# Performance work log

Hardware: AMD Instinct MI355X
Metric: run time of the kernel (lower is better)

## Reference

```python
import jax, jax.numpy as jnp
import numpy as np

DIM = 1024
D_STATE = 16
D_CONV = 4
EXPAND = 2
D_INNER = EXPAND * DIM          # 2048
DT_RANK = (DIM + 15) // 16      # 64 (math.ceil(d_model/16))
BSZ = 2
SEQ = 2048


def setup_inputs() -> dict:
    key = jax.random.key(0)
    ks = jax.random.split(key, 8)
    g = lambda k, shape, scale: (jax.random.normal(k, shape, jnp.float32) * scale)
    return {
        "x": g(ks[0], (BSZ, SEQ, DIM), 1.0),
        # in_proj: Linear(d_model -> 2*d_inner, bias=False)
        "W_in": g(ks[1], (2 * D_INNER, DIM), DIM ** -0.5),
        # depthwise causal conv1d: groups=d_inner, kernel d_conv, bias=True
        "conv_w": g(ks[2], (D_INNER, 1, D_CONV), D_CONV ** -0.5),
        "conv_b": jnp.zeros((D_INNER,), jnp.float32),
        # x_proj: Linear(d_inner -> dt_rank + 2*d_state, bias=False)
        "W_xproj": g(ks[3], (DT_RANK + 2 * D_STATE, D_INNER), D_INNER ** -0.5),
        # dt_proj: Linear(dt_rank -> d_inner, bias=True)
        "W_dt": g(ks[4], (D_INNER, DT_RANK), DT_RANK ** -0.5),
        "b_dt": g(ks[5], (D_INNER,), 0.1),
        # S4D-real init: A = -exp(A_log), A_log = log(1..d_state)
        "A_log": jnp.log(jnp.broadcast_to(
            jnp.arange(1, D_STATE + 1, dtype=jnp.float32), (D_INNER, D_STATE))),
        "D": jnp.ones((D_INNER,), jnp.float32),
        # out_proj: Linear(d_inner -> d_model, bias=False)
        "W_out": g(ks[6], (DIM, D_INNER), D_INNER ** -0.5),
        # wrapper LayerNorm(dim)
        "gamma": jnp.ones((DIM,), jnp.float32),
        "beta": jnp.zeros((DIM,), jnp.float32),
    }


def reference(x, W_in, conv_w, conv_b, W_xproj, W_dt, b_dt,
              A_log, D, W_out, gamma, beta):
    B, L, _ = x.shape
    # ---- input projection, split into conv path and gate ----
    xz = x @ W_in.T                              # (B, L, 2*d_inner)
    xc, z = jnp.split(xz, 2, axis=-1)
    # ---- depthwise causal conv1d + SiLU ----
    xt = jnp.transpose(xc, (0, 2, 1))            # (B, d_inner, L)
    conv = jax.lax.conv_general_dilated(
        xt, conv_w, window_strides=(1,), padding=[(D_CONV - 1, 0)],
        dimension_numbers=("NCH", "OIH", "NCH"), feature_group_count=D_INNER)
    u = jax.nn.silu(jnp.transpose(conv + conv_b[None, :, None], (0, 2, 1)))  # (B,L,d_inner)
    # ---- input-dependent delta, B, C ----
    xdbc = u @ W_xproj.T                          # (B, L, dt_rank + 2*d_state)
    dt = xdbc[..., :DT_RANK]
    Bm = xdbc[..., DT_RANK:DT_RANK + D_STATE]     # (B, L, d_state)
    Cm = xdbc[..., DT_RANK + D_STATE:]            # (B, L, d_state)
    delta = jax.nn.softplus(dt @ W_dt.T + b_dt)   # (B, L, d_inner)
    A = -jnp.exp(A_log)                           # (d_inner, d_state)
    # ---- selective scan: h_t = exp(dt*A) h_{t-1} + dt*B_t*u_t ; y_t = <h_t, C_t> ----
    def step(h, inputs):
        d_t, u_t, B_t, C_t = inputs               # (B,d_inner),(B,d_inner),(B,S),(B,S)
        dA = jnp.exp(d_t[:, :, None] * A)         # (B, d_inner, S)
        h = h * dA + (d_t * u_t)[:, :, None] * B_t[:, None, :]
        y = jnp.einsum("bds,bs->bd", h, C_t)
        return h, y
    tm = lambda a: jnp.transpose(a, (1, 0, 2))    # time-major for scan
    h0 = jnp.zeros((B, D_INNER, D_STATE), x.dtype)
    _, ys = jax.lax.scan(step, h0, (tm(delta), tm(u), tm(Bm), tm(Cm)))
    y = jnp.transpose(ys, (1, 0, 2)) + u * D      # skip term D*u
    y = y * jax.nn.silu(z)                        # gate
    out = y @ W_out.T                             # (B, L, dim)
    # ---- wrapper LayerNorm(dim), eps=1e-5 ----
    mean = out.mean(-1, keepdims=True)
    var = out.var(-1, keepdims=True)
    return (out - mean) * jax.lax.rsqrt(var + 1e-5) * gamma + beta
```

## Files before the change

kernel.cpp:

```cpp
#include <hip/hip_runtime.h>
#include <stdint.h>

typedef unsigned short u16;
typedef __bf16 bf16x8 __attribute__((ext_vector_type(8)));
typedef unsigned short u16x8 __attribute__((ext_vector_type(8)));
typedef unsigned short u16x4 __attribute__((ext_vector_type(4)));
typedef float f32x4 __attribute__((ext_vector_type(4)));

#define BSZ 2
#define SEQ 2048
#define DIM 1024
#define D_INNER 2048
#define DT_RANK 64
#define D_STATE 16
#define XPROJ_N 96
#define NCHUNK 32
#define CHUNK_T 64
#define LOG2E 1.44269504f

#define N_X   4194304
#define N_W   4194304
#define N_WX  196608
#define N_WDT 131072
#define N_WO  2097152
#define N_XD  393216

__device__ __forceinline__ float bf2f(u16 h) {
    return __uint_as_float(((unsigned)h) << 16);
}
__device__ __forceinline__ u16 f2bf(float f) {
    unsigned u = __float_as_uint(f);
    unsigned r = (u + 0x7FFFu + ((u >> 16) & 1u)) >> 16;
    return (u16)r;
}

__device__ __forceinline__ f32x4 mfma16(bf16x8 a, bf16x8 b, f32x4 c) {
    return __builtin_amdgcn_mfma_f32_16x16x32_bf16(a, b, c, 0, 0, 0);
}

__device__ __forceinline__ void gload_lds16(const void* g, void* l) {
    __builtin_amdgcn_global_load_lds(
        (const __attribute__((address_space(1))) unsigned int*)(uintptr_t)g,
        (__attribute__((address_space(3))) unsigned int*)(uintptr_t)l,
        16, 0, 0);
}

__device__ __forceinline__ void split4(const float* __restrict__ in,
                                       u16* __restrict__ hi, u16* __restrict__ lo,
                                       long i)
{
    f32x4 v = *(const f32x4*)(in + i);
    u16x4 h, l;
    #pragma unroll
    for (int j = 0; j < 4; j++) {
        u16 hh = f2bf(v[j]);
        h[j] = hh;
        l[j] = f2bf(v[j] - bf2f(hh));
    }
    *(u16x4*)(hi + i) = h;
    *(u16x4*)(lo + i) = l;
}

__global__ __launch_bounds__(256)
void megasplit4(const float* __restrict__ x,  u16* __restrict__ xh,  u16* __restrict__ xl,
                const float* __restrict__ w,  u16* __restrict__ wh,  u16* __restrict__ wl,
                const float* __restrict__ wx, u16* __restrict__ wxh, u16* __restrict__ wxl,
                const float* __restrict__ wd, u16* __restrict__ wdh, u16* __restrict__ wdl)
{
    long i = ((long)blockIdx.x * 256 + threadIdx.x) * 4;
    if (i < N_X) { split4(x, xh, xl, i); return; }
    i -= N_X;
    if (i < N_W) { split4(w, wh, wl, i); return; }
    i -= N_W;
    if (i < N_WX) { split4(wx, wxh, wxl, i); return; }
    i -= N_WX;
    if (i < N_WDT) { split4(wd, wdh, wdl, i); }
}

#define PH_TOP                                                                \
    __builtin_amdgcn_sched_barrier(0);                                        \
    __builtin_amdgcn_s_barrier();                                             \
    asm volatile("s_waitcnt lgkmcnt(0)" ::: "memory");                        \
    __builtin_amdgcn_sched_barrier(0);                                        \
    __builtin_amdgcn_s_setprio(1);
#define PH_BOT                                                                \
    __builtin_amdgcn_s_setprio(0);                                            \
    __builtin_amdgcn_sched_barrier(0);                                        \
    __builtin_amdgcn_s_barrier();

__global__ __launch_bounds__(512, 2)
void gemm256_xz(const u16* __restrict__ xh, const u16* __restrict__ xl,
                const u16* __restrict__ wh, const u16* __restrict__ wl,
                u16* __restrict__ xc, float* __restrict__ z)
{
    __shared__ u16 lds[65536];

    const int tid  = threadIdx.x;
    const int w    = tid >> 6;
    const int lane = tid & 63;
    const int r16  = lane & 15;
    const int quad = lane >> 4;
    const int wr   = w >> 2;
    const int wc   = w & 3;
    const long m0  = (long)blockIdx.y * 256;
    const long n0  = (long)blockIdx.x * 256;

    const int c0 = tid, c1 = tid + 512;
    const int ma0 = c0 >> 2, kc0 = ((c0 & 3) ^ ((ma0 >> 1) & 3)) * 8;
    const int ma1 = c1 >> 2, kc1 = ((c1 & 3) ^ ((ma1 >> 1) & 3)) * 8;
    const int arow0 = ((int)m0 + ma0) * DIM + kc0;
    const int arow1 = ((int)m0 + ma1) * DIM + kc1;
    const int brow0 = ((int)n0 + ma0) * DIM + kc0;
    const int brow1 = ((int)n0 + ma1) * DIM + kc1;

    int caof[8], cbof[4];
    #pragma unroll
    for (int i = 0; i < 8; i++) {
        int m = wr * 128 + i * 16 + r16;
        caof[i] = (m * 4 + (quad ^ ((m >> 1) & 3))) * 8;
    }
    #pragma unroll
    for (int j = 0; j < 4; j++) {
        int n = wc * 64 + j * 16 + r16;
        cbof[j] = (n * 4 + (quad ^ ((n >> 1) & 3))) * 8;
    }

    f32x4 acc[8][4];
    #pragma unroll
    for (int i = 0; i < 8; i++)
        #pragma unroll
        for (int j = 0; j < 4; j++) acc[i][j] = {0.f, 0.f, 0.f, 0.f};

    gload_lds16(xh + arow0, lds + c0 * 8);
    gload_lds16(xh + arow1, lds + c1 * 8);
    gload_lds16(xl + arow0, lds + 8192 + c0 * 8);
    gload_lds16(xl + arow1, lds + 8192 + c1 * 8);
    gload_lds16(wh + brow0, lds + 16384 + c0 * 8);
    gload_lds16(wh + brow1, lds + 16384 + c1 * 8);
    gload_lds16(wl + brow0, lds + 24576 + c0 * 8);
    gload_lds16(wl + brow1, lds + 24576 + c1 * 8);
    asm volatile("s_waitcnt vmcnt(0)" ::: "memory");
    __builtin_amdgcn_s_barrier();

    int kt = 0;
#define XZ_FTILE(CUR, SN)                                                     \
  {                                                                           \
    int st = kt + 1; if (st > 31) st = 31;                                    \
    const int kb = st * 32;                                                   \
    const u16* AHp = lds + (CUR) * 32768;                                     \
    const u16* ALp = AHp + 8192;                                              \
    const u16* BHp = AHp + 16384;                                             \
    const u16* BLp = AHp + 24576;                                             \
    u16* Sb = lds + (SN) * 32768;                                             \
    bf16x8 a0[4], a1[4], fb[4];                                               \
                            \
    _Pragma("unroll") for (int j = 0; j < 4; j++)                             \
        fb[j] = *(const bf16x8*)(BHp + cbof[j]);                              \
    _Pragma("unroll") for (int i = 0; i < 4; i++)                             \
        a0[i] = *(const bf16x8*)(AHp + caof[i]);                              \
    gload_lds16(xh + arow0 + kb, Sb + c0 * 8);                                \
    gload_lds16(xh + arow1 + kb, Sb + c1 * 8);                                \
    PH_TOP                                                                    \
    _Pragma("unroll") for (int i = 0; i < 4; i++)                             \
      _Pragma("unroll") for (int j = 0; j < 4; j++)                           \
        acc[i][j] = mfma16(a0[i], fb[j], acc[i][j]);                          \
    PH_BOT                                                                    \
                                \
    _Pragma("unroll") for (int i = 0; i < 4; i++)                             \
        a1[i] = *(const bf16x8*)(AHp + caof[4 + i]);                          \
    gload_lds16(xl + arow0 + kb, Sb + 8192 + c0 * 8);                         \
    gload_lds16(xl + arow1 + kb, Sb + 8192 + c1 * 8);                         \
    PH_TOP                                                                    \
    _Pragma("unroll") for (int i = 0; i < 4; i++)                             \
      _Pragma("unroll") for (int j = 0; j < 4; j++)                           \
        acc[4 + i][j] = mfma16(a1[i], fb[j], acc[4 + i][j]);                  \
    PH_BOT                                                                    \
                        \
    _Pragma("unroll") for (int j = 0; j < 4; j++)                             \
        fb[j] = *(const bf16x8*)(BLp + cbof[j]);                              \
    gload_lds16(wh + brow0 + kb, Sb + 16384 + c0 * 8);                        \
    gload_lds16(wh + brow1 + kb, Sb + 16384 + c1 * 8);                        \
    PH_TOP                                                                    \
    _Pragma("unroll") for (int i = 0; i < 4; i++)                             \
      _Pragma("unroll") for (int j = 0; j < 4; j++)                           \
        acc[i][j] = mfma16(a0[i], fb[j], acc[i][j]);                          \
    PH_BOT                                                                    \
                             \
    gload_lds16(wl + brow0 + kb, Sb + 24576 + c0 * 8);                        \
    gload_lds16(wl + brow1 + kb, Sb + 24576 + c1 * 8);                        \
    PH_TOP                                                                    \
    _Pragma("unroll") for (int i = 0; i < 4; i++)                             \
      _Pragma("unroll") for (int j = 0; j < 4; j++)                           \
        acc[4 + i][j] = mfma16(a1[i], fb[j], acc[4 + i][j]);                  \
    PH_BOT                                                                    \
                              \
    _Pragma("unroll") for (int j = 0; j < 4; j++)                             \
        fb[j] = *(const bf16x8*)(BHp + cbof[j]);                              \
    _Pragma("unroll") for (int i = 0; i < 4; i++)                             \
        a0[i] = *(const bf16x8*)(ALp + caof[i]);                              \
    PH_TOP                                                                    \
    _Pragma("unroll") for (int i = 0; i < 4; i++)                             \
      _Pragma("unroll") for (int j = 0; j < 4; j++)                           \
        acc[i][j] = mfma16(a0[i], fb[j], acc[i][j]);                          \
    PH_BOT                                                                    \
                 \
    _Pragma("unroll") for (int i = 0; i < 4; i++)                             \
        a1[i] = *(const bf16x8*)(ALp + caof[4 + i]);                          \
    PH_TOP                                                                    \
    _Pragma("unroll") for (int i = 0; i < 4; i++)                             \
      _Pragma("unroll") for (int j = 0; j < 4; j++)                           \
        acc[4 + i][j] = mfma16(a1[i], fb[j], acc[4 + i][j]);                  \
    __builtin_amdgcn_s_setprio(0);                                            \
    __builtin_amdgcn_sched_barrier(0);                                        \
    asm volatile("s_waitcnt vmcnt(0)" ::: "memory");                          \
    __builtin_amdgcn_s_barrier();                                             \
    kt++;                                                                     \
  }

    #pragma unroll 1
    for (int it = 0; it < 16; it++) {
        XZ_FTILE(0, 1)
        XZ_FTILE(1, 0)
    }
#undef XZ_FTILE

    asm volatile("s_waitcnt vmcnt(0)" ::: "memory");

    const bool isz = (n0 >= 2048);
    #pragma unroll
    for (int i = 0; i < 8; i++) {
        #pragma unroll
        for (int j = 0; j < 4; j++) {
            long col = n0 + wc * 64 + j * 16 + r16;
            #pragma unroll
            for (int r = 0; r < 4; r++) {
                long row = m0 + wr * 128 + i * 16 + quad * 4 + r;
                if (!isz) xc[row * (long)D_INNER + col] = f2bf(acc[i][j][r]);
                else      z[row * (long)D_INNER + (col - D_INNER)] = acc[i][j][r];
            }
        }
    }
}

__global__ __launch_bounds__(512, 2)
void gemm256_out(const u16* __restrict__ A, const u16* __restrict__ Bh,
                 const u16* __restrict__ Bl, float* __restrict__ OutBase)
{
    __shared__ u16 lds[49152];

    const int tid  = threadIdx.x;
    const int w    = tid >> 6;
    const int lane = tid & 63;
    const int r16  = lane & 15;
    const int quad = lane >> 4;
    const int wr   = w >> 2;
    const int wc   = w & 3;
    const long m0  = (long)blockIdx.y * 256;
    const long n0  = (long)blockIdx.x * 256;
    const int  kz  = blockIdx.z;
    const u16* Bs  = (kz >= 2) ? Bl : Bh;
    const int  kbase = (kz & 1) * 1024;
    float* Out = OutBase + (long)kz * 4194304;

    const int c0 = tid, c1 = tid + 512;
    const int ma0 = c0 >> 2, kc0 = ((c0 & 3) ^ ((ma0 >> 1) & 3)) * 8;
    const int ma1 = c1 >> 2, kc1 = ((c1 & 3) ^ ((ma1 >> 1) & 3)) * 8;
    const int arow0 = ((int)m0 + ma0) * D_INNER + kbase + kc0;
    const int arow1 = ((int)m0 + ma1) * D_INNER + kbase + kc1;
    const int brow0 = ((int)n0 + ma0) * D_INNER + kbase + kc0;
    const int brow1 = ((int)n0 + ma1) * D_INNER + kbase + kc1;

    int caof[8], cbof[4];
    #pragma unroll
    for (int i = 0; i < 8; i++) {
        int m = wr * 128 + i * 16 + r16;
        caof[i] = (m * 4 + (quad ^ ((m >> 1) & 3))) * 8;
    }
    #pragma unroll
    for (int j = 0; j < 4; j++) {
        int n = wc * 64 + j * 16 + r16;
        cbof[j] = (n * 4 + (quad ^ ((n >> 1) & 3))) * 8;
    }

    f32x4 acc[8][4];
    #pragma unroll
    for (int i = 0; i < 8; i++)
        #pragma unroll
        for (int j = 0; j < 4; j++) acc[i][j] = {0.f, 0.f, 0.f, 0.f};

    gload_lds16(A  + arow0,      lds + c0 * 8);
    gload_lds16(A  + arow1,      lds + c1 * 8);
    gload_lds16(Bs + brow0,      lds + 24576 + c0 * 8);
    gload_lds16(Bs + brow1,      lds + 24576 + c1 * 8);
    gload_lds16(A  + arow0 + 32, lds + 8192 + c0 * 8);
    gload_lds16(A  + arow1 + 32, lds + 8192 + c1 * 8);
    gload_lds16(Bs + brow0 + 32, lds + 24576 + 8192 + c0 * 8);
    gload_lds16(Bs + brow1 + 32, lds + 24576 + 8192 + c1 * 8);
    asm volatile("s_waitcnt vmcnt(4)" ::: "memory");
    __builtin_amdgcn_s_barrier();

    int kt = 0;
#define OUT_ITER(CUR, SL)                                                     \
  {                                                                           \
    int st = kt + 2; if (st > 31) st = 31;                                    \
    const int kb = st * 32;                                                   \
    const u16* Alds = lds + (CUR) * 8192;                                     \
    const u16* Blds = lds + 24576 + (CUR) * 8192;                             \
    bf16x8 bfr[4], afr[4];                                                    \
    _Pragma("unroll") for (int j = 0; j < 4; j++)                             \
        bfr[j] = *(const bf16x8*)(Blds + cbof[j]);                            \
    _Pragma("unroll") for (int i = 0; i < 4; i++)                             \
        afr[i] = *(const bf16x8*)(Alds + caof[i]);                            \
    gload_lds16(A + arow0 + kb, lds + (SL) * 8192 + c0 * 8);                  \
    gload_lds16(A + arow1 + kb, lds + (SL) * 8192 + c1 * 8);                  \
    PH_TOP                                                                    \
    _Pragma("unroll") for (int i = 0; i < 4; i++)                             \
      _Pragma("unroll") for (int j = 0; j < 4; j++)                           \
        acc[i][j] = mfma16(afr[i], bfr[j], acc[i][j]);                        \
    PH_BOT                                                                    \
    bf16x8 af2[4];                                                            \
    _Pragma("unroll") for (int i = 0; i < 4; i++)                             \
        af2[i] = *(const bf16x8*)(Alds + caof[4 + i]);                        \
    gload_lds16(Bs + brow0 + kb, lds + 24576 + (SL) * 8192 + c0 * 8);         \
    gload_lds16(Bs + brow1 + kb, lds + 24576 + (SL) * 8192 + c1 * 8);         \
    PH_TOP                                                                    \
    _Pragma("unroll") for (int i = 0; i < 4; i++)                             \
      _Pragma("unroll") for (int j = 0; j < 4; j++)                           \
        acc[4 + i][j] = mfma16(af2[i], bfr[j], acc[4 + i][j]);                \
    __builtin_amdgcn_s_setprio(0);                                            \
    __builtin_amdgcn_sched_barrier(0);                                        \
    asm volatile("s_waitcnt vmcnt(4)" ::: "memory");                          \
    __builtin_amdgcn_s_barrier();                                             \
    kt++;                                                                     \
  }

    #pragma unroll 1
    for (int it = 0; it < 10; it++) {
        OUT_ITER(0, 2)
        OUT_ITER(1, 0)
        OUT_ITER(2, 1)
    }
    OUT_ITER(0, 2)
    OUT_ITER(1, 0)
#undef OUT_ITER

    asm volatile("s_waitcnt vmcnt(0)" ::: "memory");

    #pragma unroll
    for (int i = 0; i < 8; i++) {
        #pragma unroll
        for (int j = 0; j < 4; j++) {
            long col = n0 + wc * 64 + j * 16 + r16;
            #pragma unroll
            for (int r = 0; r < 4; r++) {
                long row = m0 + wr * 128 + i * 16 + quad * 4 + r;
                Out[row * (long)DIM + col] = acc[i][j][r];
            }
        }
    }
}

__global__ __launch_bounds__(64)
void gemm_dt32(const u16* __restrict__ Ah, const u16* __restrict__ Al, int lda,
               const u16* __restrict__ Bh, const u16* __restrict__ Bl, int ldb,
               float* __restrict__ C, int ldc, const float* __restrict__ bias)
{
    const int lane = threadIdx.x;
    const int r16  = lane & 15;
    const int quad = lane >> 4;
    const long m0 = (long)blockIdx.y * 32;
    const long n0 = (long)blockIdx.x * 32;

    const u16* Ah0 = Ah + (m0 + r16) * (long)lda + quad * 8;
    const u16* Ah1 = Ah0 + 16L * lda;
    const u16* Al0 = Al + (m0 + r16) * (long)lda + quad * 8;
    const u16* Al1 = Al0 + 16L * lda;
    const u16* Bh0 = Bh + (n0 + r16) * (long)ldb + quad * 8;
    const u16* Bh1 = Bh0 + 16L * ldb;
    const u16* Bl0 = Bl + (n0 + r16) * (long)ldb + quad * 8;
    const u16* Bl1 = Bl0 + 16L * ldb;

    f32x4 acc00 = {0,0,0,0}, acc01 = {0,0,0,0}, acc10 = {0,0,0,0}, acc11 = {0,0,0,0};

    #pragma unroll
    for (int k = 0; k < DT_RANK; k += 32) {
        bf16x8 a0h = *(const bf16x8*)(Ah0 + k);
        bf16x8 a1h = *(const bf16x8*)(Ah1 + k);
        bf16x8 a0l = *(const bf16x8*)(Al0 + k);
        bf16x8 a1l = *(const bf16x8*)(Al1 + k);
        bf16x8 b0h = *(const bf16x8*)(Bh0 + k);
        bf16x8 b1h = *(const bf16x8*)(Bh1 + k);
        bf16x8 b0l = *(const bf16x8*)(Bl0 + k);
        bf16x8 b1l = *(const bf16x8*)(Bl1 + k);
        acc00 = mfma16(a0h, b0h, acc00); acc00 = mfma16(a0h, b0l, acc00); acc00 = mfma16(a0l, b0h, acc00);
        acc01 = mfma16(a0h, b1h, acc01); acc01 = mfma16(a0h, b1l, acc01); acc01 = mfma16(a0l, b1h, acc01);
        acc10 = mfma16(a1h, b0h, acc10); acc10 = mfma16(a1h, b0l, acc10); acc10 = mfma16(a1l, b0h, acc10);
        acc11 = mfma16(a1h, b1h, acc11); acc11 = mfma16(a1h, b1l, acc11); acc11 = mfma16(a1l, b1h, acc11);
    }

    #pragma unroll
    for (int i = 0; i < 2; i++) {
        #pragma unroll
        for (int j = 0; j < 2; j++) {
            f32x4 v = (i == 0) ? (j == 0 ? acc00 : acc01) : (j == 0 ? acc10 : acc11);
            long col = n0 + j * 16 + r16;
            #pragma unroll
            for (int r = 0; r < 4; r++) {
                long row = m0 + i * 16 + quad * 4 + r;
                float x = v[r] + bias[col];
                x = (x > 15.f) ? x : log1pf(__expf(x));
                C[row * (long)ldc + col] = x;
            }
        }
    }
}

__global__ __launch_bounds__(64)
void gemm3_skp(const u16* __restrict__ A, int lda,
               const u16* __restrict__ Bh, const u16* __restrict__ Bl, int ldb,
               float* __restrict__ Cpart, int ldc, int K0)
{
    const int lane = threadIdx.x;
    const int r16  = lane & 15;
    const int quad = lane >> 4;
    const long m0 = (long)blockIdx.y * 32;
    const long n0 = (long)blockIdx.x * 32;
    const int kbase = blockIdx.z * K0;
    float* C = Cpart + (long)blockIdx.z * N_XD;

    const u16* Ap0 = A  + (m0 + r16) * (long)lda + quad * 8 + kbase;
    const u16* Ap1 = Ap0 + 16L * lda;
    const u16* Bh0 = Bh + (n0 + r16) * (long)ldb + quad * 8 + kbase;
    const u16* Bh1 = Bh0 + 16L * ldb;
    const u16* Bl0 = Bl + (n0 + r16) * (long)ldb + quad * 8 + kbase;
    const u16* Bl1 = Bl0 + 16L * ldb;

    f32x4 acc00 = {0,0,0,0}, acc01 = {0,0,0,0}, acc10 = {0,0,0,0}, acc11 = {0,0,0,0};

    for (int k = 0; k < K0; k += 32) {
        bf16x8 a0 = *(const bf16x8*)(Ap0 + k);
        bf16x8 a1 = *(const bf16x8*)(Ap1 + k);
        bf16x8 b0h = *(const bf16x8*)(Bh0 + k);
        bf16x8 b1h = *(const bf16x8*)(Bh1 + k);
        bf16x8 b0l = *(const bf16x8*)(Bl0 + k);
        bf16x8 b1l = *(const bf16x8*)(Bl1 + k);
        acc00 = mfma16(a0, b0h, acc00); acc00 = mfma16(a0, b0l, acc00);
        acc01 = mfma16(a0, b1h, acc01); acc01 = mfma16(a0, b1l, acc01);
        acc10 = mfma16(a1, b0h, acc10); acc10 = mfma16(a1, b0l, acc10);
        acc11 = mfma16(a1, b1h, acc11); acc11 = mfma16(a1, b1l, acc11);
    }

    #pragma unroll
    for (int i = 0; i < 2; i++) {
        #pragma unroll
        for (int j = 0; j < 2; j++) {
            f32x4 v = (i == 0) ? (j == 0 ? acc00 : acc01) : (j == 0 ? acc10 : acc11);
            long col = n0 + j * 16 + r16;
            #pragma unroll
            for (int r = 0; r < 4; r++) {
                long row = m0 + i * 16 + quad * 4 + r;
                C[row * (long)ldc + col] = v[r];
            }
        }
    }
}

__global__ __launch_bounds__(256)
void combine3(const float* __restrict__ part, float* __restrict__ xdbc,
              u16* __restrict__ hi, u16* __restrict__ lo)
{
    long i = ((long)blockIdx.x * 256 + threadIdx.x) * 4;
    if (i >= N_XD) return;
    f32x4 s = *(const f32x4*)(part + i);
    #pragma unroll
    for (int j = 1; j < 8; j++) {
        f32x4 p = *(const f32x4*)(part + (long)j * N_XD + i);
        s[0] += p[0]; s[1] += p[1]; s[2] += p[2]; s[3] += p[3];
    }
    *(f32x4*)(xdbc + i) = s;
    u16x4 h, l;
    #pragma unroll
    for (int j = 0; j < 4; j++) {
        u16 hh = f2bf(s[j]);
        h[j] = hh;
        l[j] = f2bf(s[j] - bf2f(hh));
    }
    *(u16x4*)(hi + i) = h;
    *(u16x4*)(lo + i) = l;
}

__global__ __launch_bounds__(256)
void conv_silu(const u16* __restrict__ xc, const float* __restrict__ cw,
               const float* __restrict__ cb, u16* __restrict__ u)
{
    long idx = ((long)blockIdx.x * 256 + threadIdx.x) * 8;
    int t  = (int)((idx >> 11) & 2047);
    int d0 = (int)(idx & 2047);

    bf16x8 xrow[4];
    #pragma unroll
    for (int j = 0; j < 4; j++) {
        int tt = t - 3 + j;
        if (tt >= 0) xrow[j] = *(const bf16x8*)(xc + idx + (long)(j - 3) * D_INNER);
        else         xrow[j] = bf16x8{0,0,0,0,0,0,0,0};
    }
    u16x8 out;
    #pragma unroll
    for (int e = 0; e < 8; e++) {
        int d = d0 + e;
        float acc = cb[d];
        #pragma unroll
        for (int j = 0; j < 4; j++)
            acc += cw[d * 4 + j] * (float)xrow[j][e];
        out[e] = f2bf(acc / (1.f + __expf(-acc)));
    }
    *(u16x8*)(u + idx) = out;
}

__global__ __launch_bounds__(256)
void scan_partA(const float* __restrict__ delta, const u16* __restrict__ u,
                const float* __restrict__ xdbc, const float* __restrict__ A_log,
                float* __restrict__ hbuf, float* __restrict__ sdelta,
                const float* __restrict__ wout, u16* __restrict__ wouth,
                u16* __restrict__ woutl)
{
    const int d = blockIdx.x * 256 + threadIdx.x;
    const int c = blockIdx.y;
    const int b = blockIdx.z;
    const int t0 = c * CHUNK_T;

    float Af[16];
    #pragma unroll
    for (int s = 0; s < 16; s++) Af[s] = -__expf(A_log[d * 16 + s]) * LOG2E;
    bool fast = true;
    #pragma unroll
    for (int s = 0; s < 16; s++)
        fast = fast && (fabsf(Af[s] - (float)(s + 1) * Af[0]) < 1e-3f * (float)(s + 1));

    float h[16];
    #pragma unroll
    for (int s = 0; s < 16; s++) h[s] = 0.f;
    float sd = 0.f;

    const float* dptr = delta + ((long)b * SEQ + t0) * D_INNER + d;
    const u16*   uptr = u     + ((long)b * SEQ + t0) * D_INNER + d;
    const float* xp   = xdbc  + ((long)b * SEQ + t0) * XPROJ_N;

    if (fast) {
        const float Af0 = Af[0];
        for (int t = 0; t < CHUNK_T; t++) {
            float dl = dptr[(long)t * D_INNER];
            float uu = bf2f(uptr[(long)t * D_INNER]);
            f32x4 B0 = *(const f32x4*)(xp + t * XPROJ_N + DT_RANK);
            f32x4 B1 = *(const f32x4*)(xp + t * XPROJ_N + DT_RANK + 4);
            f32x4 B2 = *(const f32x4*)(xp + t * XPROJ_N + DT_RANK + 8);
            f32x4 B3 = *(const f32x4*)(xp + t * XPROJ_N + DT_RANK + 12);
            float Bv[16] = {B0[0],B0[1],B0[2],B0[3], B1[0],B1[1],B1[2],B1[3],
                            B2[0],B2[1],B2[2],B2[3], B3[0],B3[1],B3[2],B3[3]};
            sd += dl;
            float dlu = dl * uu;
            float q = exp2f(dl * Af0);
            float dAc = 1.f;
            #pragma unroll
            for (int s = 0; s < 16; s++) {
                dAc *= q;
                h[s] = h[s] * dAc + dlu * Bv[s];
            }
        }
    } else {
        for (int t = 0; t < CHUNK_T; t++) {
            float dl = dptr[(long)t * D_INNER];
            float uu = bf2f(uptr[(long)t * D_INNER]);
            f32x4 B0 = *(const f32x4*)(xp + t * XPROJ_N + DT_RANK);
            f32x4 B1 = *(const f32x4*)(xp + t * XPROJ_N + DT_RANK + 4);
            f32x4 B2 = *(const f32x4*)(xp + t * XPROJ_N + DT_RANK + 8);
            f32x4 B3 = *(const f32x4*)(xp + t * XPROJ_N + DT_RANK + 12);
            float Bv[16] = {B0[0],B0[1],B0[2],B0[3], B1[0],B1[1],B1[2],B1[3],
                            B2[0],B2[1],B2[2],B2[3], B3[0],B3[1],B3[2],B3[3]};
            sd += dl;
            float dlu = dl * uu;
            #pragma unroll
            for (int s = 0; s < 16; s++)
                h[s] = h[s] * exp2f(dl * Af[s]) + dlu * Bv[s];
        }
    }

    float* hout = hbuf + ((long)(b * NCHUNK + c) * D_INNER + d) * 16;
    #pragma unroll
    for (int s = 0; s < 16; s++) hout[s] = h[s];
    sdelta[(long)(b * NCHUNK + c) * D_INNER + d] = sd;

    long tidg = (((long)b * NCHUNK + c) * 8 + blockIdx.x) * 256 + threadIdx.x;
    long base = tidg * 16;
    #pragma unroll
    for (int k = 0; k < 4; k++) split4(wout, wouth, woutl, base + 4 * k);
}

__global__ __launch_bounds__(256)
void scan_fixup(float* __restrict__ hbuf, const float* __restrict__ sdelta,
                const float* __restrict__ A_log)
{
    const int idx = blockIdx.x * 256 + threadIdx.x;
    const int ds = idx & (D_INNER * 16 - 1);
    const int b  = idx >> 15;
    const float Af = -__expf(A_log[ds]) * LOG2E;
    float hin = 0.f;
    #pragma unroll 4
    for (int c = 0; c < NCHUNK; c++) {
        long gi = (long)(b * NCHUNK + c) * (D_INNER * 16) + ds;
        float e = hbuf[gi];
        hbuf[gi] = hin;
        float sd = sdelta[(long)(b * NCHUNK + c) * D_INNER + (ds >> 4)];
        hin = e + exp2f(Af * sd) * hin;
    }
}

__global__ __launch_bounds__(256)
void scan_partC(const float* __restrict__ delta, const u16* __restrict__ u,
                const float* __restrict__ xdbc, const float* __restrict__ z,
                const float* __restrict__ A_log, const float* __restrict__ Dp,
                const float* __restrict__ hbuf, u16* __restrict__ y)
{
    const int d = blockIdx.x * 256 + threadIdx.x;
    const int c = blockIdx.y;
    const int b = blockIdx.z;
    const int t0 = c * CHUNK_T;

    float Af[16];
    #pragma unroll
    for (int s = 0; s < 16; s++) Af[s] = -__expf(A_log[d * 16 + s]) * LOG2E;
    bool fast = true;
    #pragma unroll
    for (int s = 0; s < 16; s++)
        fast = fast && (fabsf(Af[s] - (float)(s + 1) * Af[0]) < 1e-3f * (float)(s + 1));
    const float Dd = Dp[d];

    float h[16];
    const float* hin = hbuf + ((long)(b * NCHUNK + c) * D_INNER + d) * 16;
    #pragma unroll
    for (int s = 0; s < 16; s++) h[s] = hin[s];

    const float* dptr = delta + ((long)b * SEQ + t0) * D_INNER + d;
    const u16*   uptr = u     + ((long)b * SEQ + t0) * D_INNER + d;
    const float* zptr = z     + ((long)b * SEQ + t0) * D_INNER + d;
    const float* xp   = xdbc  + ((long)b * SEQ + t0) * XPROJ_N;
    u16* yptr = y + ((long)b * SEQ + t0) * D_INNER + d;

    if (fast) {
        const float Af0 = Af[0];
        for (int t = 0; t < CHUNK_T; t++) {
            float dl = dptr[(long)t * D_INNER];
            float uu = bf2f(uptr[(long)t * D_INNER]);
            float zl = zptr[(long)t * D_INNER];
            f32x4 B0 = *(const f32x4*)(xp + t * XPROJ_N + DT_RANK);
            f32x4 B1 = *(const f32x4*)(xp + t * XPROJ_N + DT_RANK + 4);
            f32x4 B2 = *(const f32x4*)(xp + t * XPROJ_N + DT_RANK + 8);
            f32x4 B3 = *(const f32x4*)(xp + t * XPROJ_N + DT_RANK + 12);
            f32x4 C0 = *(const f32x4*)(xp + t * XPROJ_N + DT_RANK + 16);
            f32x4 C1 = *(const f32x4*)(xp + t * XPROJ_N + DT_RANK + 20);
            f32x4 C2 = *(const f32x4*)(xp + t * XPROJ_N + DT_RANK + 24);
            f32x4 C3 = *(const f32x4*)(xp + t * XPROJ_N + DT_RANK + 28);
            float Bv[16] = {B0[0],B0[1],B0[2],B0[3], B1[0],B1[1],B1[2],B1[3],
                            B2[0],B2[1],B2[2],B2[3], B3[0],B3[1],B3[2],B3[3]};
            float Cv[16] = {C0[0],C0[1],C0[2],C0[3], C1[0],C1[1],C1[2],C1[3],
                            C2[0],C2[1],C2[2],C2[3], C3[0],C3[1],C3[2],C3[3]};
            float dlu = dl * uu;
            float q = exp2f(dl * Af0);
            float dAc = 1.f;
            float p0 = 0.f, p1 = 0.f, p2 = 0.f, p3 = 0.f;
            #pragma unroll
            for (int s = 0; s < 16; s += 4) {
                float dA0 = dAc * q;
                float dA1 = dA0 * q;
                float dA2 = dA1 * q;
                float dA3 = dA2 * q;
                dAc = dA3;
                h[s]   = h[s]   * dA0 + dlu * Bv[s];
                h[s+1] = h[s+1] * dA1 + dlu * Bv[s+1];
                h[s+2] = h[s+2] * dA2 + dlu * Bv[s+2];
                h[s+3] = h[s+3] * dA3 + dlu * Bv[s+3];
                p0 += h[s]   * Cv[s];
                p1 += h[s+1] * Cv[s+1];
                p2 += h[s+2] * Cv[s+2];
                p3 += h[s+3] * Cv[s+3];
            }
            float acc = (p0 + p1) + (p2 + p3);
            float sz = zl / (1.f + __expf(-zl));
            float yy = (acc + uu * Dd) * sz;
            yptr[(long)t * D_INNER] = f2bf(yy);
        }
    } else {
        for (int t = 0; t < CHUNK_T; t++) {
            float dl = dptr[(long)t * D_INNER];
            float uu = bf2f(uptr[(long)t * D_INNER]);
            float zl = zptr[(long)t * D_INNER];
            f32x4 B0 = *(const f32x4*)(xp + t * XPROJ_N + DT_RANK);
            f32x4 B1 = *(const f32x4*)(xp + t * XPROJ_N + DT_RANK + 4);
            f32x4 B2 = *(const f32x4*)(xp + t * XPROJ_N + DT_RANK + 8);
            f32x4 B3 = *(const f32x4*)(xp + t * XPROJ_N + DT_RANK + 12);
            f32x4 C0 = *(const f32x4*)(xp + t * XPROJ_N + DT_RANK + 16);
            f32x4 C1 = *(const f32x4*)(xp + t * XPROJ_N + DT_RANK + 20);
            f32x4 C2 = *(const f32x4*)(xp + t * XPROJ_N + DT_RANK + 24);
            f32x4 C3 = *(const f32x4*)(xp + t * XPROJ_N + DT_RANK + 28);
            float Bv[16] = {B0[0],B0[1],B0[2],B0[3], B1[0],B1[1],B1[2],B1[3],
                            B2[0],B2[1],B2[2],B2[3], B3[0],B3[1],B3[2],B3[3]};
            float Cv[16] = {C0[0],C0[1],C0[2],C0[3], C1[0],C1[1],C1[2],C1[3],
                            C2[0],C2[1],C2[2],C2[3], C3[0],C3[1],C3[2],C3[3]};
            float dlu = dl * uu;
            float p0 = 0.f, p1 = 0.f, p2 = 0.f, p3 = 0.f;
            #pragma unroll
            for (int s = 0; s < 16; s += 4) {
                h[s]   = h[s]   * exp2f(dl * Af[s])   + dlu * Bv[s];
                h[s+1] = h[s+1] * exp2f(dl * Af[s+1]) + dlu * Bv[s+1];
                h[s+2] = h[s+2] * exp2f(dl * Af[s+2]) + dlu * Bv[s+2];
                h[s+3] = h[s+3] * exp2f(dl * Af[s+3]) + dlu * Bv[s+3];
                p0 += h[s]   * Cv[s];
                p1 += h[s+1] * Cv[s+1];
                p2 += h[s+2] * Cv[s+2];
                p3 += h[s+3] * Cv[s+3];
            }
            float acc = (p0 + p1) + (p2 + p3);
            float sz = zl / (1.f + __expf(-zl));
            float yy = (acc + uu * Dd) * sz;
            yptr[(long)t * D_INNER] = f2bf(yy);
        }
    }
}

__global__ __launch_bounds__(256)
void layernorm_kernel(const float* __restrict__ p0,
                      const float* __restrict__ gamma, const float* __restrict__ beta,
                      float* __restrict__ out)
{
    const long row = blockIdx.x;
    const long base = row * DIM;
    int tid = threadIdx.x;
    float v[4];
    float sum = 0.f, sq = 0.f;
    #pragma unroll
    for (int i = 0; i < 4; i++) {
        long c = base + tid + i * 256;
        v[i] = (p0[c] + p0[c + 4194304]) + (p0[c + 8388608] + p0[c + 12582912]);
        sum += v[i];
        sq  += v[i] * v[i];
    }
    #pragma unroll
    for (int off = 1; off < 64; off <<= 1) {
        sum += __shfl_xor(sum, off);
        sq  += __shfl_xor(sq, off);
    }
    __shared__ float ssum[4], ssq[4];
    int w = tid >> 6;
    if ((tid & 63) == 0) { ssum[w] = sum; ssq[w] = sq; }
    __syncthreads();
    float ts = ssum[0] + ssum[1] + ssum[2] + ssum[3];
    float tq = ssq[0] + ssq[1] + ssq[2] + ssq[3];
    float mean = ts * (1.f / DIM);
    float var  = tq * (1.f / DIM) - mean * mean;
    float rstd = rsqrtf(var + 1e-5f);
    float* o = out + base;
    #pragma unroll
    for (int i = 0; i < 4; i++) {
        int c = tid + i * 256;
        o[c] = (v[i] - mean) * rstd * gamma[c] + beta[c];
    }
}

extern "C" void kernel_launch(void* const* d_in, const int* in_sizes, int n_in,
                              void* d_out, int out_size, void* d_ws, size_t ws_size,
                              hipStream_t stream)
{
    const float* x      = (const float*)d_in[0];
    const float* W_in   = (const float*)d_in[1];
    const float* conv_w = (const float*)d_in[2];
    const float* conv_b = (const float*)d_in[3];
    const float* W_xproj= (const float*)d_in[4];
    const float* W_dt   = (const float*)d_in[5];
    const float* b_dt   = (const float*)d_in[6];
    const float* A_log  = (const float*)d_in[7];
    const float* Dv     = (const float*)d_in[8];
    const float* W_out  = (const float*)d_in[9];
    const float* gamma  = (const float*)d_in[10];
    const float* beta   = (const float*)d_in[11];

    char* ws = (char*)d_ws;
    u16*   xc    = (u16*)(ws);
    float* g3p   = (float*)(ws);
    u16*   xdh   = (u16*)(ws + 12582912);
    u16*   xdl   = (u16*)(ws + 14155776);
    float* hbuf  = (float*)(ws);
    u16*   wouth = (u16*)(ws + 8388608);
    u16*   woutl = (u16*)(ws + 12582912);
    float* z     = (float*)(ws + 16777216);
    float* opre  = (float*)(ws + 16777216);
    u16*   u     = (u16*)(ws + 50331648);
    u16*   xh    = (u16*)(ws + 67108864);
    u16*   xl    = (u16*)(ws + 75497472);
    u16*   wh    = (u16*)(ws + 83886080);
    u16*   wl    = (u16*)(ws + 92274688);
    float* delta = (float*)(ws + 67108864);
    float* xdbc  = (float*)(ws + 100663296);
    u16*   wxh   = (u16*)(ws + 102236160);
    u16*   wxl   = (u16*)(ws + 102629376);
    u16*   wdth  = (u16*)(ws + 103022592);
    u16*   wdtl  = (u16*)(ws + 103284736);
    float* sdel  = (float*)(ws + 103546880);
    u16*   yb    = (u16*)d_out;

    megasplit4<<<8512, 256, 0, stream>>>(x, xh, xl, W_in, wh, wl,
                                         W_xproj, wxh, wxl, W_dt, wdth, wdtl);
    gemm256_xz<<<dim3(16, 16), 512, 0, stream>>>(xh, xl, wh, wl, xc, z);
    conv_silu<<<4096, 256, 0, stream>>>(xc, conv_w, conv_b, u);
    gemm3_skp<<<dim3(3, 128, 8), 64, 0, stream>>>(
        u, D_INNER, wxh, wxl, D_INNER, g3p, XPROJ_N, 256);
    combine3<<<384, 256, 0, stream>>>(g3p, xdbc, xdh, xdl);
    gemm_dt32<<<dim3(64, 128), 64, 0, stream>>>(
        xdh, xdl, XPROJ_N, wdth, wdtl, DT_RANK, delta, D_INNER, b_dt);
    scan_partA<<<dim3(8, NCHUNK, BSZ), 256, 0, stream>>>(
        delta, u, xdbc, A_log, hbuf, sdel, W_out, wouth, woutl);
    scan_fixup<<<256, 256, 0, stream>>>(hbuf, sdel, A_log);
    scan_partC<<<dim3(8, NCHUNK, BSZ), 256, 0, stream>>>(delta, u, xdbc, z, A_log, Dv, hbuf, yb);
    gemm256_out<<<dim3(4, 16, 4), 512, 0, stream>>>(yb, wouth, woutl, opre);
    layernorm_kernel<<<4096, 256, 0, stream>>>(opre, gamma, beta, (float*)d_out);
}
```

Baseline: 391.6 us.

## Restructure out-projection GEMM to share A tile across hi/lo weight halves

The out-projection GEMM previously split K and the hi/lo bf16 weight halves across four z-slices, each loading its own A tile and writing a separate partial sum. It now uses 128-row tiles with two K-split slices, loads the A tile once per stage, and applies it against both Bh and Bl, so A traffic drops and only two partials need summing in LayerNorm. The pipeline depth goes from three stages to two with full vmcnt waits. In the xz GEMM, the hi/lo B fragments are kept in separate registers to avoid reloading Bh from LDS, at the cost of extra VGPRs.

```diff
diff --git a/kernel.cpp b/kernel.cpp
--- a/kernel.cpp
+++ b/kernel.cpp
@@ -152,10 +152,10 @@
     const u16* BHp = AHp + 16384;                                             \
     const u16* BLp = AHp + 24576;                                             \
     u16* Sb = lds + (SN) * 32768;                                             \
-    bf16x8 a0[4], a1[4], fb[4];                                               \
+    bf16x8 a0[4], a1[4], fbh[4], fbl[4];                                      \
                             \
     _Pragma("unroll") for (int j = 0; j < 4; j++)                             \
-        fb[j] = *(const bf16x8*)(BHp + cbof[j]);                              \
+        fbh[j] = *(const bf16x8*)(BHp + cbof[j]);                             \
     _Pragma("unroll") for (int i = 0; i < 4; i++)                             \
         a0[i] = *(const bf16x8*)(AHp + caof[i]);                              \
     gload_lds16(xh + arow0 + kb, Sb + c0 * 8);                                \
@@ -163,7 +163,7 @@
     PH_TOP                                                                    \
     _Pragma("unroll") for (int i = 0; i < 4; i++)                             \
       _Pragma("unroll") for (int j = 0; j < 4; j++)                           \
-        acc[i][j] = mfma16(a0[i], fb[j], acc[i][j]);                          \
+        acc[i][j] = mfma16(a0[i], fbh[j], acc[i][j]);                         \
     PH_BOT                                                                    \
                                 \
     _Pragma("unroll") for (int i = 0; i < 4; i++)                             \
@@ -173,17 +173,17 @@
     PH_TOP                                                                    \
     _Pragma("unroll") for (int i = 0; i < 4; i++)                             \
       _Pragma("unroll") for (int j = 0; j < 4; j++)                           \
-        acc[4 + i][j] = mfma16(a1[i], fb[j], acc[4 + i][j]);                  \
+        acc[4 + i][j] = mfma16(a1[i], fbh[j], acc[4 + i][j]);                 \
     PH_BOT                                                                    \
                         \
     _Pragma("unroll") for (int j = 0; j < 4; j++)                             \
-        fb[j] = *(const bf16x8*)(BLp + cbof[j]);                              \
+        fbl[j] = *(const bf16x8*)(BLp + cbof[j]);                             \
     gload_lds16(wh + brow0 + kb, Sb + 16384 + c0 * 8);                        \
     gload_lds16(wh + brow1 + kb, Sb + 16384 + c1 * 8);                        \
     PH_TOP                                                                    \
     _Pragma("unroll") for (int i = 0; i < 4; i++)                             \
       _Pragma("unroll") for (int j = 0; j < 4; j++)                           \
-        acc[i][j] = mfma16(a0[i], fb[j], acc[i][j]);                          \
+        acc[i][j] = mfma16(a0[i], fbl[j], acc[i][j]);                         \
     PH_BOT                                                                    \
                              \
     gload_lds16(wl + brow0 + kb, Sb + 24576 + c0 * 8);                        \
@@ -191,25 +191,23 @@
     PH_TOP                                                                    \
     _Pragma("unroll") for (int i = 0; i < 4; i++)                             \
       _Pragma("unroll") for (int j = 0; j < 4; j++)                           \
-        acc[4 + i][j] = mfma16(a1[i], fb[j], acc[4 + i][j]);                  \
+        acc[4 + i][j] = mfma16(a1[i], fbl[j], acc[4 + i][j]);                 \
     PH_BOT                                                                    \
-                              \
-    _Pragma("unroll") for (int j = 0; j < 4; j++)                             \
-        fb[j] = *(const bf16x8*)(BHp + cbof[j]);                              \
+                   \
     _Pragma("unroll") for (int i = 0; i < 4; i++)                             \
         a0[i] = *(const bf16x8*)(ALp + caof[i]);                              \
     PH_TOP                                                                    \
     _Pragma("unroll") for (int i = 0; i < 4; i++)                             \
       _Pragma("unroll") for (int j = 0; j < 4; j++)                           \
-        acc[i][j] = mfma16(a0[i], fb[j], acc[i][j]);                          \
+        acc[i][j] = mfma16(a0[i], fbh[j], acc[i][j]);                         \
     PH_BOT                                                                    \
-                 \
+                      \
     _Pragma("unroll") for (int i = 0; i < 4; i++)                             \
         a1[i] = *(const bf16x8*)(ALp + caof[4 + i]);                          \
     PH_TOP                                                                    \
     _Pragma("unroll") for (int i = 0; i < 4; i++)                             \
       _Pragma("unroll") for (int j = 0; j < 4; j++)                           \
-        acc[4 + i][j] = mfma16(a1[i], fb[j], acc[4 + i][j]);                  \
+        acc[4 + i][j] = mfma16(a1[i], fbh[j], acc[4 + i][j]);                 \
     __builtin_amdgcn_s_setprio(0);                                            \
     __builtin_amdgcn_sched_barrier(0);                                        \
     asm volatile("s_waitcnt vmcnt(0)" ::: "memory");                          \
@@ -246,7 +244,7 @@
 void gemm256_out(const u16* __restrict__ A, const u16* __restrict__ Bh,
                  const u16* __restrict__ Bl, float* __restrict__ OutBase)
 {
-    __shared__ u16 lds[49152];
+    __shared__ u16 lds[40960];
 
     const int tid  = threadIdx.x;
     const int w    = tid >> 6;
@@ -255,25 +253,24 @@
     const int quad = lane >> 4;
     const int wr   = w >> 2;
     const int wc   = w & 3;
-    const long m0  = (long)blockIdx.y * 256;
+    const long m0  = (long)blockIdx.y * 128;
     const long n0  = (long)blockIdx.x * 256;
     const int  kz  = blockIdx.z;
-    const u16* Bs  = (kz >= 2) ? Bl : Bh;
-    const int  kbase = (kz & 1) * 1024;
+    const int  kbase = kz * 1024;
     float* Out = OutBase + (long)kz * 4194304;
 
+    const int maA = tid >> 2, kcA = ((tid & 3) ^ ((maA >> 1) & 3)) * 8;
+    const int arow = ((int)m0 + maA) * D_INNER + kbase + kcA;
     const int c0 = tid, c1 = tid + 512;
-    const int ma0 = c0 >> 2, kc0 = ((c0 & 3) ^ ((ma0 >> 1) & 3)) * 8;
-    const int ma1 = c1 >> 2, kc1 = ((c1 & 3) ^ ((ma1 >> 1) & 3)) * 8;
-    const int arow0 = ((int)m0 + ma0) * D_INNER + kbase + kc0;
-    const int arow1 = ((int)m0 + ma1) * D_INNER + kbase + kc1;
-    const int brow0 = ((int)n0 + ma0) * D_INNER + kbase + kc0;
-    const int brow1 = ((int)n0 + ma1) * D_INNER + kbase + kc1;
-
-    int caof[8], cbof[4];
-    #pragma unroll
-    for (int i = 0; i < 8; i++) {
-        int m = wr * 128 + i * 16 + r16;
+    const int mb0 = c0 >> 2, kb0 = ((c0 & 3) ^ ((mb0 >> 1) & 3)) * 8;
+    const int mb1 = c1 >> 2, kb1 = ((c1 & 3) ^ ((mb1 >> 1) & 3)) * 8;
+    const int brow0 = ((int)n0 + mb0) * D_INNER + kbase + kb0;
+    const int brow1 = ((int)n0 + mb1) * D_INNER + kbase + kb1;
+
+    int caof[4], cbof[4];
+    #pragma unroll
+    for (int i = 0; i < 4; i++) {
+        int m = wr * 64 + i * 16 + r16;
         caof[i] = (m * 4 + (quad ^ ((m >> 1) & 3))) * 8;
     }
     #pragma unroll
@@ -282,78 +279,76 @@
         cbof[j] = (n * 4 + (quad ^ ((n >> 1) & 3))) * 8;
     }
 
-    f32x4 acc[8][4];
-    #pragma unroll
-    for (int i = 0; i < 8; i++)
+    f32x4 acc[4][4];
+    #pragma unroll
+    for (int i = 0; i < 4; i++)
         #pragma unroll
         for (int j = 0; j < 4; j++) acc[i][j] = {0.f, 0.f, 0.f, 0.f};
 
-    gload_lds16(A  + arow0,      lds + c0 * 8);
-    gload_lds16(A  + arow1,      lds + c1 * 8);
-    gload_lds16(Bs + brow0,      lds + 24576 + c0 * 8);
-    gload_lds16(Bs + brow1,      lds + 24576 + c1 * 8);
-    gload_lds16(A  + arow0 + 32, lds + 8192 + c0 * 8);
-    gload_lds16(A  + arow1 + 32, lds + 8192 + c1 * 8);
-    gload_lds16(Bs + brow0 + 32, lds + 24576 + 8192 + c0 * 8);
-    gload_lds16(Bs + brow1 + 32, lds + 24576 + 8192 + c1 * 8);
-    asm volatile("s_waitcnt vmcnt(4)" ::: "memory");
+    gload_lds16(A  + arow,  lds + tid * 8);
+    gload_lds16(Bh + brow0, lds + 4096 + c0 * 8);
+    gload_lds16(Bh + brow1, lds + 4096 + c1 * 8);
+    gload_lds16(Bl + brow0, lds + 12288 + c0 * 8);
+    gload_lds16(Bl + brow1, lds + 12288 + c1 * 8);
+    asm volatile("s_waitcnt vmcnt(0)" ::: "memory");
     __builtin_amdgcn_s_barrier();
 
     int kt = 0;
-#define OUT_ITER(CUR, SL)                                                     \
+#define O2_TILE(CUR, SN)                                                      \
   {                                                                           \
-    int st = kt + 2; if (st > 31) st = 31;                                    \
+    int st = kt + 1; if (st > 31) st = 31;                                    \
     const int kb = st * 32;                                                   \
-    const u16* Alds = lds + (CUR) * 8192;                                     \
-    const u16* Blds = lds + 24576 + (CUR) * 8192;                             \
-    bf16x8 bfr[4], afr[4];                                                    \
+    const u16* Ap  = lds + (CUR) * 20480;                                     \
+    const u16* BHp = Ap + 4096;                                               \
+    const u16* BLp = Ap + 12288;                                              \
+    u16* Sb = lds + (SN) * 20480;                                             \
+    bf16x8 fa[4], fb[4];                                                      \
+                            \
     _Pragma("unroll") for (int j = 0; j < 4; j++)                             \
-        bfr[j] = *(const bf16x8*)(Blds + cbof[j]);                            \
-    _Pragma("unroll") for (int i = 0; i < 4; i++)                             \
-        afr[i] = *(const bf16x8*)(Alds + caof[i]);                            \
-    gload_lds16(A + arow0 + kb, lds + (SL) * 8192 + c0 * 8);                  \
-    gload_lds16(A + arow1 + kb, lds + (SL) * 8192 + c1 * 8);                  \
+        fb[j] = *(const bf16x8*)(BHp + cbof[j]);                              \
+    _Pragma("unroll") for (int i = 0; i < 4; i++)                             \
+        fa[i] = *(const bf16x8*)(Ap + caof[i]);                               \
+    gload_lds16(A + arow + kb, Sb + tid * 8);                                 \
     PH_TOP                                                                    \
     _Pragma("unroll") for (int i = 0; i < 4; i++)                             \
       _Pragma("unroll") for (int j = 0; j < 4; j++)                           \
-        acc[i][j] = mfma16(afr[i], bfr[j], acc[i][j]);                        \
+        acc[i][j] = mfma16(fa[i], fb[j], acc[i][j]);                          \
     PH_BOT                                                                    \
-    bf16x8 af2[4];                                                            \
-    _Pragma("unroll") for (int i = 0; i < 4; i++)                             \
-        af2[i] = *(const bf16x8*)(Alds + caof[4 + i]);                        \
-    gload_lds16(Bs + brow0 + kb, lds + 24576 + (SL) * 8192 + c0 * 8);         \
-    gload_lds16(Bs + brow1 + kb, lds + 24576 + (SL) * 8192 + c1 * 8);         \
+                 \
+    _Pragma("unroll") for (int j = 0; j < 4; j++)                             \
+        fb[j] = *(const bf16x8*)(BLp + cbof[j]);                              \
+    gload_lds16(Bh + brow0 + kb, Sb + 4096 + c0 * 8);                         \
+    gload_lds16(Bh + brow1 + kb, Sb + 4096 + c1 * 8);                         \
+    gload_lds16(Bl + brow0 + kb, Sb + 12288 + c0 * 8);                        \
+    gload_lds16(Bl + brow1 + kb, Sb + 12288 + c1 * 8);                        \
     PH_TOP                                                                    \
     _Pragma("unroll") for (int i = 0; i < 4; i++)                             \
       _Pragma("unroll") for (int j = 0; j < 4; j++)                           \
-        acc[4 + i][j] = mfma16(af2[i], bfr[j], acc[4 + i][j]);                \
+        acc[i][j] = mfma16(fa[i], fb[j], acc[i][j]);                          \
     __builtin_amdgcn_s_setprio(0);                                            \
     __builtin_amdgcn_sched_barrier(0);                                        \
-    asm volatile("s_waitcnt vmcnt(4)" ::: "memory");                          \
+    asm volatile("s_waitcnt vmcnt(0)" ::: "memory");                          \
     __builtin_amdgcn_s_barrier();                                             \
     kt++;                                                                     \
   }
 
     #pragma unroll 1
-    for (int it = 0; it < 10; it++) {
-        OUT_ITER(0, 2)
-        OUT_ITER(1, 0)
-        OUT_ITER(2, 1)
-    }
-    OUT_ITER(0, 2)
-    OUT_ITER(1, 0)
-#undef OUT_ITER
+    for (int it = 0; it < 16; it++) {
+        O2_TILE(0, 1)
+        O2_TILE(1, 0)
+    }
+#undef O2_TILE
 
     asm volatile("s_waitcnt vmcnt(0)" ::: "memory");
 
     #pragma unroll
-    for (int i = 0; i < 8; i++) {
+    for (int i = 0; i < 4; i++) {
         #pragma unroll
         for (int j = 0; j < 4; j++) {
             long col = n0 + wc * 64 + j * 16 + r16;
             #pragma unroll
             for (int r = 0; r < 4; r++) {
-                long row = m0 + wr * 128 + i * 16 + quad * 4 + r;
+                long row = m0 + wr * 64 + i * 16 + quad * 4 + r;
                 Out[row * (long)DIM + col] = acc[i][j][r];
             }
         }
@@ -740,7 +735,7 @@
     #pragma unroll
     for (int i = 0; i < 4; i++) {
         long c = base + tid + i * 256;
-        v[i] = (p0[c] + p0[c + 4194304]) + (p0[c + 8388608] + p0[c + 12582912]);
+        v[i] = p0[c] + p0[c + 4194304];
         sum += v[i];
         sq  += v[i] * v[i];
     }
@@ -820,6 +815,6 @@
         delta, u, xdbc, A_log, hbuf, sdel, W_out, wouth, woutl);
     scan_fixup<<<256, 256, 0, stream>>>(hbuf, sdel, A_log);
     scan_partC<<<dim3(8, NCHUNK, BSZ), 256, 0, stream>>>(delta, u, xdbc, z, A_log, Dv, hbuf, yb);
-    gemm256_out<<<dim3(4, 16, 4), 512, 0, stream>>>(yb, wouth, woutl, opre);
+    gemm256_out<<<dim3(4, 32, 2), 512, 0, stream>>>(yb, wouth, woutl, opre);
     layernorm_kernel<<<4096, 256, 0, stream>>>(opre, gamma, beta, (float*)d_out);
 }
```

After: 385.9 us, median of 2. No clear change (-1.5%).
